# Kernel tuning notes

Hardware: AMD Instinct MI355X
Metric: run time of the kernel (lower is better)

## Reference

```python
import jax, jax.numpy as jnp
import numpy as np
import math

B, S, E, H = 2, 2048, 1024, 16
D = E // H
# neuromodulator levels (deterministic branch choices)
NA, ACH, DA = 0.5, 0.5, -0.5

def setup_inputs() -> dict:
    key = jax.random.key(0)
    ks = jax.random.split(key, 12)
    xav = lambda k, i, o: jax.random.uniform(k, (i, o), jnp.float32, -1.0, 1.0) * math.sqrt(6.0 / (i + o))
    return {
        'query': jax.random.normal(ks[0], (B, S, E), jnp.float32),
        'key':   jax.random.normal(ks[1], (B, S, E), jnp.float32),
        'value': jax.random.normal(ks[2], (B, S, E), jnp.float32),
        'Wq': xav(ks[3], E, E), 'bq': jnp.zeros((E,), jnp.float32),
        'Wk': xav(ks[4], E, E), 'bk': jnp.zeros((E,), jnp.float32),
        'Wv': xav(ks[5], E, E), 'bv': jnp.zeros((E,), jnp.float32),
        'Wo': xav(ks[6], E, E), 'bo': jnp.zeros((E,), jnp.float32),
        'time_scales': jnp.ones((H,), jnp.float32),
    }

def reference(query, key, value, Wq, bq, Wk, bk, Wv, bv, Wo, bo, time_scales):
    # projections -> [B, H, S, D]
    q = (query @ Wq + bq).reshape(B, S, H, D).transpose(0, 2, 1, 3)
    k = (key   @ Wk + bk).reshape(B, S, H, D).transpose(0, 2, 1, 3)
    v = (value @ Wv + bv).reshape(B, S, H, D).transpose(0, 2, 1, 3)
    # per-head time-scale on keys
    k = k * time_scales[None, :, None, None]
    scores = jnp.einsum('bhtd,bhsd->bhts', q, k) / math.sqrt(D)
    # noradrenaline: temperature scaling
    temperature = 1.0 / (1.0 + NA * 0.5)
    scores = scores / temperature
    # acetylcholine: boost diagonal
    diag = jnp.eye(S, dtype=scores.dtype)[None, None]
    scores = scores * (1.0 + ACH * 0.3 * diag)
    kk = max(1, int(S * 0.2))
    topv = jax.lax.top_k(scores, kk)[0]          # [B,H,S,kk]
    min_topk = topv[..., -1:]                     # kth largest
    mask = (scores >= min_topk).astype(scores.dtype)
    scores = scores * (1.0 + (-DA) * 0.3 * mask)
    attn = jax.nn.softmax(scores, axis=-1)
    out = jnp.einsum('bhts,bhsd->bhtd', attn, v)
    out = out.transpose(0, 2, 1, 3).reshape(B, S, E)
    out = out @ Wo + bo
    return out
```

## Files before the change

### kernel.cpp

```cpp
#include <hip/hip_runtime.h>
#include <cstdint>
#include <cstddef>

#define BB 2
#define SS 2048
#define EE 1024
#define HH 16
#define DH 64
#define KKSEL 409
#define QT 16
#define PST 136

typedef __attribute__((ext_vector_type(8))) short bf16x8;
typedef __attribute__((ext_vector_type(4))) float f32x4;
typedef unsigned short ushort_t;

__device__ __forceinline__ unsigned short f2bf(float f){
    unsigned u = __float_as_uint(f);
    u += 0x7fffu + ((u >> 16) & 1u);
    return (unsigned short)(u >> 16);
}
__device__ __forceinline__ float bf2f(unsigned short h){
    return __uint_as_float(((unsigned)h) << 16);
}
__device__ __forceinline__ unsigned sortkey(float f){
    unsigned u = __float_as_uint(f);
    return (u & 0x80000000u) ? ~u : (u | 0x80000000u);
}
__device__ __forceinline__ float inv_sortkey(unsigned k){
    unsigned u = (k & 0x80000000u) ? (k & 0x7fffffffu) : ~k;
    return __uint_as_float(u);
}
__device__ __forceinline__ void split8(const float* f, bf16x8& h, bf16x8& l){
    #pragma unroll
    for (int j = 0; j < 8; ++j){
        ushort_t hh = f2bf(f[j]);
        h[j] = (short)hh;
        l[j] = (short)f2bf(f[j] - bf2f(hh));
    }
}

struct CvtArgs {
    const float* W[4];
    ushort_t* H[4];
    ushort_t* L[4];
};

__global__ __launch_bounds__(256) void convert_wt4(CvtArgs a)
{
    __shared__ float T[64][65];
    const int z = blockIdx.z;
    const float* __restrict__ W = a.W[z];
    ushort_t* __restrict__ Ht = a.H[z];
    ushort_t* __restrict__ Lt = a.L[z];

    const int tid = threadIdx.x;
    const int ty = tid >> 4, tx = tid & 15;
    const int n0 = blockIdx.x * 64, k0 = blockIdx.y * 64;
    #pragma unroll
    for (int i = 0; i < 4; ++i){
        const int kl = ty + i * 16;
        float4 w = *(const float4*)&W[(size_t)(k0 + kl) * EE + n0 + tx * 4];
        T[kl][tx*4 + 0] = w.x; T[kl][tx*4 + 1] = w.y;
        T[kl][tx*4 + 2] = w.z; T[kl][tx*4 + 3] = w.w;
    }
    __syncthreads();
    #pragma unroll
    for (int i = 0; i < 4; ++i){
        const int nl = ty + i * 16;
        ushort4 h, l;
        ushort_t* hp = &h.x; ushort_t* lp = &l.x;
        #pragma unroll
        for (int j = 0; j < 4; ++j){
            const float v = T[tx*4 + j][nl];
            ushort_t hh = f2bf(v);
            hp[j] = hh;
            lp[j] = f2bf(v - bf2f(hh));
        }
        const size_t o = (size_t)(n0 + nl) * EE + k0 + tx * 4;
        *(ushort4*)&Ht[o] = h;
        *(ushort4*)&Lt[o] = l;
    }
}

template<int MODE>
__device__ __forceinline__ void gemm_body(
        const float* __restrict__ X,
        const ushort_t* __restrict__ Wth, const ushort_t* __restrict__ Wtl,
        const float* __restrict__ bias, const float* __restrict__ ts,
        float* __restrict__ OutF, ushort_t* __restrict__ OutH,
        ushort_t* __restrict__ OutL, ushort_t* buf)
{
    const int tid  = threadIdx.x;
    const int lane = tid & 63, wave = tid >> 6;
    const int c16  = lane & 15, qd = lane >> 4;
    const int m0 = blockIdx.y * 128, n0 = blockIdx.x * 128;
    const int wm = (wave >> 1) * 64, wn = (wave & 1) * 64;
    const int lrow = tid >> 1, lkg = (tid & 1) * 16;

    f32x4 acc[4][4];
    #pragma unroll
    for (int a = 0; a < 4; ++a)
        #pragma unroll
        for (int b = 0; b < 4; ++b) acc[a][b] = (f32x4){0.f,0.f,0.f,0.f};

    const float* Xr = X + (size_t)(m0 + lrow) * EE + lkg;
    const ushort_t* Whr = Wth + (size_t)(n0 + lrow) * EE + lkg;
    const ushort_t* Wlr = Wtl + (size_t)(n0 + lrow) * EE + lkg;

    {
        float fx[16];
        *(float4*)&fx[0]  = *(const float4*)&Xr[0];
        *(float4*)&fx[4]  = *(const float4*)&Xr[4];
        *(float4*)&fx[8]  = *(const float4*)&Xr[8];
        *(float4*)&fx[12] = *(const float4*)&Xr[12];
        bf16x8 w0 = *(const bf16x8*)&Whr[0];
        bf16x8 w1 = *(const bf16x8*)&Whr[8];
        bf16x8 w2 = *(const bf16x8*)&Wlr[0];
        bf16x8 w3 = *(const bf16x8*)&Wlr[8];
        bf16x8 h0, l0, h1, l1;
        split8(fx, h0, l0); split8(fx + 8, h1, l1);
        ushort_t* S = buf;
        *(bf16x8*)&S[lrow*32 + lkg]           = h0;
        *(bf16x8*)&S[lrow*32 + lkg + 8]       = h1;
        *(bf16x8*)&S[4096 + lrow*32 + lkg]    = l0;
        *(bf16x8*)&S[4096 + lrow*32 + lkg+8]  = l1;
        *(bf16x8*)&S[8192 + lrow*32 + lkg]    = w0;
        *(bf16x8*)&S[8192 + lrow*32 + lkg+8]  = w1;
        *(bf16x8*)&S[12288 + lrow*32 + lkg]   = w2;
        *(bf16x8*)&S[12288 + lrow*32 + lkg+8] = w3;
    }
    __syncthreads();

    int cur = 0;
    for (int k0 = 0; k0 < EE; k0 += 32){
        const bool more = (k0 + 32) < EE;
        float fx[16];
        bf16x8 gw[4];
        if (more){
            const float* xp = Xr + k0 + 32;
            *(float4*)&fx[0]  = *(const float4*)&xp[0];
            *(float4*)&fx[4]  = *(const float4*)&xp[4];
            *(float4*)&fx[8]  = *(const float4*)&xp[8];
            *(float4*)&fx[12] = *(const float4*)&xp[12];
            gw[0] = *(const bf16x8*)&Whr[k0 + 32];
            gw[1] = *(const bf16x8*)&Whr[k0 + 40];
            gw[2] = *(const bf16x8*)&Wlr[k0 + 32];
            gw[3] = *(const bf16x8*)&Wlr[k0 + 40];
        }
        const ushort_t* S  = buf + cur * 16384;
        const ushort_t* A0 = S;
        const ushort_t* A1 = S + 4096;
        const ushort_t* B0 = S + 8192;
        const ushort_t* B1 = S + 12288;
        bf16x8 afh[4], afl[4], bfh[4], bfl[4];
        #pragma unroll
        for (int i = 0; i < 4; ++i){
            afh[i] = *(const bf16x8*)&A0[(wm + i*16 + c16)*32 + qd*8];
            afl[i] = *(const bf16x8*)&A1[(wm + i*16 + c16)*32 + qd*8];
            bfh[i] = *(const bf16x8*)&B0[(wn + i*16 + c16)*32 + qd*8];
            bfl[i] = *(const bf16x8*)&B1[(wn + i*16 + c16)*32 + qd*8];
        }
        #pragma unroll
        for (int a = 0; a < 4; ++a){
            #pragma unroll
            for (int b = 0; b < 4; ++b){
                if (MODE == 2){
                    acc[a][b] = __builtin_amdgcn_mfma_f32_16x16x32_bf16(afh[a], bfh[b], acc[a][b], 0,0,0);
                    acc[a][b] = __builtin_amdgcn_mfma_f32_16x16x32_bf16(afh[a], bfl[b], acc[a][b], 0,0,0);
                    acc[a][b] = __builtin_amdgcn_mfma_f32_16x16x32_bf16(afl[a], bfh[b], acc[a][b], 0,0,0);
                } else {
                    acc[a][b] = __builtin_amdgcn_mfma_f32_16x16x32_bf16(bfh[a], afh[b], acc[a][b], 0,0,0);
                    acc[a][b] = __builtin_amdgcn_mfma_f32_16x16x32_bf16(bfh[a], afl[b], acc[a][b], 0,0,0);
                    acc[a][b] = __builtin_amdgcn_mfma_f32_16x16x32_bf16(bfl[a], afh[b], acc[a][b], 0,0,0);
                }
            }
        }
        if (more){
            bf16x8 h0, l0, h1, l1;
            split8(fx, h0, l0); split8(fx + 8, h1, l1);
            ushort_t* N = buf + (cur ^ 1) * 16384;
            *(bf16x8*)&N[lrow*32 + lkg]           = h0;
            *(bf16x8*)&N[lrow*32 + lkg + 8]       = h1;
            *(bf16x8*)&N[4096 + lrow*32 + lkg]    = l0;
            *(bf16x8*)&N[4096 + lrow*32 + lkg+8]  = l1;
            *(bf16x8*)&N[8192 + lrow*32 + lkg]    = gw[0];
            *(bf16x8*)&N[8192 + lrow*32 + lkg+8]  = gw[1];
            *(bf16x8*)&N[12288 + lrow*32 + lkg]   = gw[2];
            *(bf16x8*)&N[12288 + lrow*32 + lkg+8] = gw[3];
            __syncthreads();
            cur ^= 1;
        }
    }

    if (MODE == 3){
        #pragma unroll
        for (int a = 0; a < 4; ++a){
            const int ng = n0 + wn + a*16 + qd*4;
            float4 b4 = *(const float4*)&bias[ng];
            const float bb[4] = {b4.x, b4.y, b4.z, b4.w};
            #pragma unroll
            for (int b = 0; b < 4; ++b){
                const int mg = m0 + wm + b*16 + c16;
                float4 o;
                o.x = acc[a][b][0] + bb[0]; o.y = acc[a][b][1] + bb[1];
                o.z = acc[a][b][2] + bb[2]; o.w = acc[a][b][3] + bb[3];
                *(float4*)&OutF[(size_t)mg * EE + ng] = o;
            }
        }
    } else if (MODE == 0){
        #pragma unroll
        for (int a = 0; a < 4; ++a){
            const int ng = n0 + wn + a*16 + qd*4;
            const int h = ng >> 6, d0 = ng & 63;
            float4 b4 = *(const float4*)&bias[ng];
            const float bb[4] = {b4.x, b4.y, b4.z, b4.w};
            #pragma unroll
            for (int b = 0; b < 4; ++b){
                const int mg = m0 + wm + b*16 + c16;
                const int bi = mg >> 11, s = mg & (SS - 1);
                ushort4 hv, lv;
                ushort_t* hp = &hv.x; ushort_t* lp = &lv.x;
                #pragma unroll
                for (int r = 0; r < 4; ++r){
                    const float v = acc[a][b][r] + bb[r];
                    ushort_t hh = f2bf(v);
                    hp[r] = hh;
                    lp[r] = f2bf(v - bf2f(hh));
                }
                const size_t o = (((size_t)(bi * HH + h)) * SS + s) * DH + d0;
                *(ushort4*)&OutH[o] = hv;
                *(ushort4*)&OutL[o] = lv;
            }
        }
    } else if (MODE == 1){
        #pragma unroll
        for (int a = 0; a < 4; ++a){
            const int ng = n0 + wn + a*16 + qd*4;
            const int h = ng >> 6, d0 = ng & 63;
            const float tsc = ts[h];
            float4 b4 = *(const float4*)&bias[ng];
            const float bb[4] = {b4.x, b4.y, b4.z, b4.w};
            #pragma unroll
            for (int b = 0; b < 4; ++b){
                const int mg = m0 + wm + b*16 + c16;
                const int bi = mg >> 11, s = mg & (SS - 1);
                ushort4 hv;
                ushort_t* hp = &hv.x;
                #pragma unroll
                for (int r = 0; r < 4; ++r)
                    hp[r] = f2bf((acc[a][b][r] + bb[r]) * tsc);
                *(ushort4*)&OutH[(((size_t)(bi * HH + h)) * SS + s) * DH + d0] = hv;
            }
        }
    } else {
        #pragma unroll
        for (int a = 0; a < 4; ++a){
            const int mg = m0 + wm + a*16 + qd*4;
            const int bi = mg >> 11, s0 = mg & (SS - 1);
            #pragma unroll
            for (int b = 0; b < 4; ++b){
                const int ng = n0 + wn + b*16 + c16;
                const int h = ng >> 6, d = ng & 63;
                const float bv = bias[ng];
                ushort4 hv;
                ushort_t* hp = &hv.x;
                #pragma unroll
                for (int r = 0; r < 4; ++r) hp[r] = f2bf(acc[a][b][r] + bv);
                *(ushort4*)&OutH[(((size_t)(bi * HH + h)) * DH + d) * SS + s0] = hv;
            }
        }
    }
}

__global__ __launch_bounds__(256) void gemm_qkv(
        const float* __restrict__ q, const float* __restrict__ k,
        const float* __restrict__ v,
        const ushort_t* __restrict__ Wqh, const ushort_t* __restrict__ Wql,
        const ushort_t* __restrict__ Wkh, const ushort_t* __restrict__ Wkl,
        const ushort_t* __restrict__ Wvh, const ushort_t* __restrict__ Wvl,
        const float* __restrict__ bq, const float* __restrict__ bk,
        const float* __restrict__ bv, const float* __restrict__ ts,
        ushort_t* __restrict__ Qh, ushort_t* __restrict__ Ql,
        ushort_t* __restrict__ Kh, ushort_t* __restrict__ Vth)
{
    __shared__ ushort_t buf[2 * 16384];
    const int z = blockIdx.z;
    if (z == 0)
        gemm_body<0>(q, Wqh, Wql, bq, nullptr, nullptr, Qh, Ql, buf);
    else if (z == 1)
        gemm_body<1>(k, Wkh, Wkl, bk, ts, nullptr, Kh, nullptr, buf);
    else
        gemm_body<2>(v, Wvh, Wvl, bv, nullptr, nullptr, Vth, nullptr, buf);
}

__global__ __launch_bounds__(256) void gemm_out(
        const float* __restrict__ X,
        const ushort_t* __restrict__ Wth, const ushort_t* __restrict__ Wtl,
        const float* __restrict__ bias, float* __restrict__ OutF)
{
    __shared__ ushort_t buf[2 * 16384];
    gemm_body<3>(X, Wth, Wtl, bias, nullptr, OutF, nullptr, nullptr, buf);
}

__global__ __launch_bounds__(512, 4) void attn_kernel(
        const ushort_t* __restrict__ Qh, const ushort_t* __restrict__ Ql,
        const ushort_t* __restrict__ Khi, const ushort_t* __restrict__ Vth,
        float* __restrict__ AO)
{
    __shared__ __align__(16) char uni[65536];
    __shared__ float wsums[8][16];
    __shared__ float thr16[16];

    const int tid  = threadIdx.x;
    const int lane = tid & 63;
    const int wave = tid >> 6;
    const int qd   = lane >> 4;
    const int c16  = lane & 15;
    const unsigned Bx = blockIdx.x;
    const int xcd  = Bx & 7;
    const int qq   = Bx >> 3;
    const int tile = qq & 127;
    const int bh   = (qq >> 7) * 8 + xcd;
    const int t0   = tile * QT;
    const int wbase = wave * 256;

    bf16x8 qh[2], ql[2];
    {
        const size_t qbase = ((size_t)bh * SS + t0 + c16) * DH;
        #pragma unroll
        for (int kc = 0; kc < 2; ++kc){
            qh[kc] = *(const bf16x8*)&Qh[qbase + kc*32 + qd*8];
            ql[kc] = *(const bf16x8*)&Ql[qbase + kc*32 + qd*8];
        }
    }

    f32x4 acc[16];
    const ushort_t* Kh = Khi + (size_t)bh * SS * DH;
    #pragma unroll
    for (int t = 0; t < 16; ++t){
        f32x4 a = {0.f, 0.f, 0.f, 0.f};
        const int srow = wbase + t*16 + c16;
        const ushort_t* kp = Kh + (size_t)srow * DH + qd*8;
        #pragma unroll
        for (int kc = 0; kc < 2; ++kc){
            bf16x8 kh = *(const bf16x8*)(kp + kc*32);
            a = __builtin_amdgcn_mfma_f32_16x16x32_bf16(qh[kc], kh, a, 0, 0, 0);
            a = __builtin_amdgcn_mfma_f32_16x16x32_bf16(ql[kc], kh, a, 0, 0, 0);
        }
        acc[t] = a;
    }

    #pragma unroll
    for (int t = 0; t < 16; ++t){
        const int colg = wbase + t*16 + c16;
        #pragma unroll
        for (int r = 0; r < 4; ++r){
            float v = acc[t][r] * 0.15625f;
            if (colg == t0 + qd*4 + r) v *= 1.15f;
            acc[t][r] = v;
        }
    }

    float* ex = (float*)uni;
    #pragma unroll
    for (int half = 0; half < 2; ++half){
        if ((qd >> 1) == half){
            const int rl = (qd & 1) * 4;
            #pragma unroll
            for (int t = 0; t < 16; ++t)
                #pragma unroll
                for (int r = 0; r < 4; ++r)
                    ex[(rl + r) * SS + wbase + t*16 + c16] = acc[t][r];
        }
        __syncthreads();
        float cand[32];
        #pragma unroll
        for (int j = 0; j < 32; ++j)
            cand[j] = ex[wave * SS + lane + 64*j];
        float mx = cand[0], mn = cand[0];
        #pragma unroll
        for (int j = 1; j < 32; ++j){
            mx = fmaxf(mx, cand[j]);
            mn = fminf(mn, cand[j]);
        }
        #pragma unroll
        for (int off = 1; off < 64; off <<= 1){
            mx = fmaxf(mx, __shfl_xor(mx, off, 64));
            mn = fminf(mn, __shfl_xor(mn, off, 64));
        }
        unsigned lo = sortkey(mn), hi = sortkey(mx) + 1u;
        #pragma unroll 1
        for (int it = 0; it < 32 && (hi - lo) > 1u; ++it){
            const unsigned mid = lo + ((hi - lo) >> 1);
            const float midf = inv_sortkey(mid);
            int c = 0;
            #pragma unroll
            for (int j = 0; j < 32; ++j)
                c += (int)__popcll(__ballot(cand[j] >= midf));
            if (c == KKSEL){ lo = mid; break; }
            if (c > KKSEL) lo = mid; else hi = mid;
        }
        if (lane == 0) thr16[half*8 + wave] = inv_sortkey(lo);
        __syncthreads();
    }

    float thr[4];
    #pragma unroll
    for (int r = 0; r < 4; ++r) thr[r] = thr16[qd*4 + r];
    float psum[4] = {0.f, 0.f, 0.f, 0.f};
    #pragma unroll
    for (int t = 0; t < 16; ++t){
        #pragma unroll
        for (int r = 0; r < 4; ++r){
            float s = acc[t][r];
            s *= (s >= thr[r]) ? 1.15f : 1.0f;
            const float e = __expf(s);
            acc[t][r] = e;
            psum[r] += e;
        }
    }
    #pragma unroll
    for (int off = 1; off <= 8; off <<= 1){
        #pragma unroll
        for (int r = 0; r < 4; ++r) psum[r] += __shfl_xor(psum[r], off, 64);
    }
    if (c16 == 0){
        #pragma unroll
        for (int r = 0; r < 4; ++r) wsums[wave][qd*4 + r] = psum[r];
    }
    __syncthreads();
    float pinv[4];
    #pragma unroll
    for (int r = 0; r < 4; ++r){
        const int row = qd*4 + r;
        float s = 0.f;
        #pragma unroll
        for (int w = 0; w < 8; ++w) s += wsums[w][row];
        pinv[r] = 1.f / s;
    }

    const ushort_t* Vh = Vth + (size_t)bh * DH * SS;
    ushort_t* pw = (ushort_t*)uni + wave * (QT * PST);
    f32x4 oacc[4];
    #pragma unroll
    for (int dt = 0; dt < 4; ++dt) oacc[dt] = (f32x4){0.f, 0.f, 0.f, 0.f};

    #pragma unroll
    for (int half = 0; half < 2; ++half){
        #pragma unroll
        for (int tt = 0; tt < 8; ++tt){
            const int t = half*8 + tt;
            #pragma unroll
            for (int r = 0; r < 4; ++r)
                pw[(qd*4 + r) * PST + tt*16 + c16] = f2bf(acc[t][r] * pinv[r]);
        }
        #pragma unroll
        for (int kc = 0; kc < 4; ++kc){
            bf16x8 pf = *(const bf16x8*)&pw[c16 * PST + kc*32 + qd*8];
            const int sbase = wbase + half*128 + kc*32 + qd*8;
            #pragma unroll
            for (int dt = 0; dt < 4; ++dt){
                const int d = dt*16 + c16;
                bf16x8 vh = *(const bf16x8*)(Vh + (size_t)d * SS + sbase);
                oacc[dt] = __builtin_amdgcn_mfma_f32_16x16x32_bf16(pf, vh, oacc[dt], 0, 0, 0);
            }
        }
    }

    __syncthreads();
    float* red = (float*)uni;
    #pragma unroll
    for (int dt = 0; dt < 4; ++dt)
        #pragma unroll
        for (int r = 0; r < 4; ++r)
            red[(wave*16 + qd*4 + r) * 65 + dt*16 + c16] = oacc[dt][r];
    __syncthreads();

    const int b = bh >> 4, h = bh & 15;
    {
        const int r  = tid >> 5;
        const int c2 = (tid & 31) * 2;
        float s0 = 0.f, s1 = 0.f;
        #pragma unroll
        for (int w = 0; w < 8; ++w){
            s0 += red[(w*16 + r) * 65 + c2];
            s1 += red[(w*16 + r) * 65 + c2 + 1];
        }
        float2 o; o.x = s0; o.y = s1;
        *(float2*)&AO[((size_t)b * SS + t0 + r) * EE + h*DH + c2] = o;
    }
}

extern "C" void kernel_launch(void* const* d_in, const int* in_sizes, int n_in,
                              void* d_out, int out_size, void* d_ws, size_t ws_size,
                              hipStream_t stream)
{
    const float* query = (const float*)d_in[0];
    const float* key   = (const float*)d_in[1];
    const float* value = (const float*)d_in[2];
    const float* Wq    = (const float*)d_in[3];
    const float* bq    = (const float*)d_in[4];
    const float* Wk    = (const float*)d_in[5];
    const float* bk    = (const float*)d_in[6];
    const float* Wv    = (const float*)d_in[7];
    const float* bv    = (const float*)d_in[8];
    const float* Wo    = (const float*)d_in[9];
    const float* bo    = (const float*)d_in[10];
    const float* ts    = (const float*)d_in[11];
    float* out = (float*)d_out;
    char* w = (char*)d_ws;

    const size_t MB = 1u << 20;
    ushort_t* Qh  = (ushort_t*)(w + 0 * MB);
    ushort_t* Ql  = (ushort_t*)(w + 8 * MB);
    ushort_t* Kh  = (ushort_t*)(w + 16 * MB);
    ushort_t* Vth = (ushort_t*)(w + 24 * MB);
    float*    AOw = (float*)   (w + 32 * MB);
    ushort_t* Wqh = (ushort_t*)(w + 32 * MB);
    ushort_t* Wql = (ushort_t*)(w + 34 * MB);
    ushort_t* Wkh = (ushort_t*)(w + 36 * MB);
    ushort_t* Wkl = (ushort_t*)(w + 38 * MB);
    ushort_t* Wvh = (ushort_t*)(w + 40 * MB);
    ushort_t* Wvl = (ushort_t*)(w + 42 * MB);
    ushort_t* Woh = (ushort_t*)(w + 48 * MB);
    ushort_t* Wol = (ushort_t*)(w + 50 * MB);

    CvtArgs ca;
    ca.W[0] = Wq;  ca.W[1] = Wk;  ca.W[2] = Wv;  ca.W[3] = Wo;
    ca.H[0] = Wqh; ca.H[1] = Wkh; ca.H[2] = Wvh; ca.H[3] = Woh;
    ca.L[0] = Wql; ca.L[1] = Wkl; ca.L[2] = Wvl; ca.L[3] = Wol;

    hipLaunchKernelGGL(convert_wt4, dim3(16, 16, 4), dim3(256), 0, stream, ca);
    hipLaunchKernelGGL(gemm_qkv, dim3(8, 32, 3), dim3(256), 0, stream,
                       query, key, value, Wqh, Wql, Wkh, Wkl, Wvh, Wvl,
                       bq, bk, bv, ts, Qh, Ql, Kh, Vth);
    hipLaunchKernelGGL(attn_kernel, dim3(BB * HH * (SS / QT)), dim3(512), 0, stream,
                       Qh, Ql, Kh, Vth, AOw);
    hipLaunchKernelGGL(gemm_out, dim3(8, 32), dim3(256), 0, stream,
                       AOw, Woh, Wol, bo, out);
}
```

Baseline: 656.4 us.

## Use 4-way radix search for top-k threshold, fold scale into Q, add setprio

The top-k threshold search now tests three pivots per iteration instead of one, so each pass splits the range four ways and needs fewer iterations and ballot rounds. The 1/sqrt(D)*temperature scale moves into the Q projection epilogue, and the diagonal boost runs only in the wave that owns the diagonal. The two score-row halves are staged through shared memory so the second write overlaps the first search. s_setprio wraps the MFMA loops. Risks: the iteration cap drops from 32 to 20 (each pass still narrows the range more), and the scale is now applied before the bf16 hi/lo split, which changes rounding.

```diff
diff --git a/kernel.cpp b/kernel.cpp
--- a/kernel.cpp
+++ b/kernel.cpp
@@ -38,6 +38,46 @@
         h[j] = (short)hh;
         l[j] = (short)f2bf(f[j] - bf2f(hh));
     }
+}
+
+__device__ __forceinline__ float topk_thresh(const float* cand){
+    float mx = cand[0], mn = cand[0];
+    #pragma unroll
+    for (int j = 1; j < 32; ++j){
+        mx = fmaxf(mx, cand[j]);
+        mn = fminf(mn, cand[j]);
+    }
+    #pragma unroll
+    for (int off = 1; off < 64; off <<= 1){
+        mx = fmaxf(mx, __shfl_xor(mx, off, 64));
+        mn = fminf(mn, __shfl_xor(mn, off, 64));
+    }
+    unsigned lo = sortkey(mn), hi = sortkey(mx) + 1u;
+    #pragma unroll 1
+    for (int it = 0; it < 20 && (hi - lo) > 1u; ++it){
+        const unsigned span = hi - lo;
+        const unsigned p1 = lo + (span >> 2);
+        const unsigned p2 = lo + (span >> 1);
+        const unsigned p3 = p2 + (span >> 2);
+        const float f1 = inv_sortkey(p1);
+        const float f2 = inv_sortkey(p2);
+        const float f3 = inv_sortkey(p3);
+        int c1 = 0, c2 = 0, c3 = 0;
+        #pragma unroll
+        for (int j = 0; j < 32; ++j){
+            c1 += (int)__popcll(__ballot(cand[j] >= f1));
+            c2 += (int)__popcll(__ballot(cand[j] >= f2));
+            c3 += (int)__popcll(__ballot(cand[j] >= f3));
+        }
+        if (c1 == KKSEL){ lo = p1; break; }
+        if (c2 == KKSEL){ lo = p2; break; }
+        if (c3 == KKSEL){ lo = p3; break; }
+        if (c1 < KKSEL)       hi = p1;
+        else if (c2 < KKSEL){ lo = p1; hi = p2; }
+        else if (c3 < KKSEL){ lo = p2; hi = p3; }
+        else                  lo = p3;
+    }
+    return inv_sortkey(lo);
 }
 
 struct CvtArgs {
@@ -161,6 +201,7 @@
             bfh[i] = *(const bf16x8*)&B0[(wn + i*16 + c16)*32 + qd*8];
             bfl[i] = *(const bf16x8*)&B1[(wn + i*16 + c16)*32 + qd*8];
         }
+        __builtin_amdgcn_s_setprio(1);
         #pragma unroll
         for (int a = 0; a < 4; ++a){
             #pragma unroll
@@ -176,6 +217,7 @@
                 }
             }
         }
+        __builtin_amdgcn_s_setprio(0);
         if (more){
             bf16x8 h0, l0, h1, l1;
             split8(fx, h0, l0); split8(fx + 8, h1, l1);
@@ -223,7 +265,7 @@
                 ushort_t* hp = &hv.x; ushort_t* lp = &lv.x;
                 #pragma unroll
                 for (int r = 0; r < 4; ++r){
-                    const float v = acc[a][b][r] + bb[r];
+                    const float v = (acc[a][b][r] + bb[r]) * 0.15625f;
                     ushort_t hh = f2bf(v);
                     hp[r] = hh;
                     lp[r] = f2bf(v - bf2f(hh));
@@ -337,6 +379,7 @@
 
     f32x4 acc[16];
     const ushort_t* Kh = Khi + (size_t)bh * SS * DH;
+    __builtin_amdgcn_s_setprio(1);
     #pragma unroll
     for (int t = 0; t < 16; ++t){
         f32x4 a = {0.f, 0.f, 0.f, 0.f};
@@ -350,60 +393,54 @@
         }
         acc[t] = a;
     }
-
-    #pragma unroll
-    for (int t = 0; t < 16; ++t){
-        const int colg = wbase + t*16 + c16;
-        #pragma unroll
-        for (int r = 0; r < 4; ++r){
-            float v = acc[t][r] * 0.15625f;
-            if (colg == t0 + qd*4 + r) v *= 1.15f;
-            acc[t][r] = v;
+    __builtin_amdgcn_s_setprio(0);
+
+    if (wave == (t0 >> 8)){
+        #pragma unroll
+        for (int t = 0; t < 16; ++t){
+            const int colg = wbase + t*16 + c16;
+            #pragma unroll
+            for (int r = 0; r < 4; ++r)
+                if (colg == t0 + qd*4 + r) acc[t][r] *= 1.15f;
         }
     }
 
     float* ex = (float*)uni;
-    #pragma unroll
-    for (int half = 0; half < 2; ++half){
-        if ((qd >> 1) == half){
-            const int rl = (qd & 1) * 4;
-            #pragma unroll
-            for (int t = 0; t < 16; ++t)
-                #pragma unroll
-                for (int r = 0; r < 4; ++r)
-                    ex[(rl + r) * SS + wbase + t*16 + c16] = acc[t][r];
-        }
-        __syncthreads();
-        float cand[32];
-        #pragma unroll
-        for (int j = 0; j < 32; ++j)
-            cand[j] = ex[wave * SS + lane + 64*j];
-        float mx = cand[0], mn = cand[0];
-        #pragma unroll
-        for (int j = 1; j < 32; ++j){
-            mx = fmaxf(mx, cand[j]);
-            mn = fminf(mn, cand[j]);
-        }
-        #pragma unroll
-        for (int off = 1; off < 64; off <<= 1){
-            mx = fmaxf(mx, __shfl_xor(mx, off, 64));
-            mn = fminf(mn, __shfl_xor(mn, off, 64));
-        }
-        unsigned lo = sortkey(mn), hi = sortkey(mx) + 1u;
-        #pragma unroll 1
-        for (int it = 0; it < 32 && (hi - lo) > 1u; ++it){
-            const unsigned mid = lo + ((hi - lo) >> 1);
-            const float midf = inv_sortkey(mid);
-            int c = 0;
-            #pragma unroll
-            for (int j = 0; j < 32; ++j)
-                c += (int)__popcll(__ballot(cand[j] >= midf));
-            if (c == KKSEL){ lo = mid; break; }
-            if (c > KKSEL) lo = mid; else hi = mid;
-        }
-        if (lane == 0) thr16[half*8 + wave] = inv_sortkey(lo);
-        __syncthreads();
-    }
+    if (qd < 2){
+        const int rl = (qd & 1) * 4;
+        #pragma unroll
+        for (int t = 0; t < 16; ++t)
+            #pragma unroll
+            for (int r = 0; r < 4; ++r)
+                ex[(rl + r) * SS + wbase + t*16 + c16] = acc[t][r];
+    }
+    __syncthreads();
+    float cand[32];
+    #pragma unroll
+    for (int j = 0; j < 32; ++j)
+        cand[j] = ex[wave * SS + lane + 64*j];
+    __syncthreads();
+    if (qd >= 2){
+        const int rl = (qd & 1) * 4;
+        #pragma unroll
+        for (int t = 0; t < 16; ++t)
+            #pragma unroll
+            for (int r = 0; r < 4; ++r)
+                ex[(rl + r) * SS + wbase + t*16 + c16] = acc[t][r];
+    }
+    {
+        const float th0 = topk_thresh(cand);
+        if (lane == 0) thr16[wave] = th0;
+    }
+    __syncthreads();
+    #pragma unroll
+    for (int j = 0; j < 32; ++j)
+        cand[j] = ex[wave * SS + lane + 64*j];
+    {
+        const float th1 = topk_thresh(cand);
+        if (lane == 0) thr16[8 + wave] = th1;
+    }
+    __syncthreads();
 
     float thr[4];
     #pragma unroll
@@ -459,12 +496,14 @@
         for (int kc = 0; kc < 4; ++kc){
             bf16x8 pf = *(const bf16x8*)&pw[c16 * PST + kc*32 + qd*8];
             const int sbase = wbase + half*128 + kc*32 + qd*8;
+            __builtin_amdgcn_s_setprio(1);
             #pragma unroll
             for (int dt = 0; dt < 4; ++dt){
                 const int d = dt*16 + c16;
                 bf16x8 vh = *(const bf16x8*)(Vh + (size_t)d * SS + sbase);
                 oacc[dt] = __builtin_amdgcn_mfma_f32_16x16x32_bf16(pf, vh, oacc[dt], 0, 0, 0);
             }
+            __builtin_amdgcn_s_setprio(0);
         }
     }
 
```

Measured after the change: 712.2 us. 1.09x slower.

## Shrink GEMM N-tile, load weights via global_load_lds, use integer-key top-k search

Applied to the files above, without the earlier changes.

The GEMM tile drops from 128x128 to 128x64 with the grid doubled. Weight tiles now go straight to LDS through global_load_lds, and the register double-buffer is replaced by a single buffer with two barriers per k-step. This cuts LDS and register use to raise occupancy, at the cost of losing overlap between loads and MFMA. In attention, scores are stored as order-preserving integer keys. The top-k threshold bisection now uses an inline-asm unsigned compare plus popcount, starts from fixed bounds of ±64 instead of a computed min/max, and always runs 32 iterations unless it hits the exact count.

```diff
diff --git a/kernel.cpp b/kernel.cpp
--- a/kernel.cpp
+++ b/kernel.cpp
@@ -38,6 +38,11 @@
         h[j] = (short)hh;
         l[j] = (short)f2bf(f[j] - bf2f(hh));
     }
+}
+__device__ __forceinline__ void gload_lds16(const ushort_t* g, ushort_t* l){
+    __builtin_amdgcn_global_load_lds(
+        (const __attribute__((address_space(1))) void*)g,
+        (__attribute__((address_space(3))) void*)l, 16, 0, 0);
 }
 
 struct CvtArgs {
@@ -94,136 +99,113 @@
     const int tid  = threadIdx.x;
     const int lane = tid & 63, wave = tid >> 6;
     const int c16  = lane & 15, qd = lane >> 4;
-    const int m0 = blockIdx.y * 128, n0 = blockIdx.x * 128;
-    const int wm = (wave >> 1) * 64, wn = (wave & 1) * 64;
+    const int m0 = blockIdx.y * 128, n0 = blockIdx.x * 64;
+    const int wm = (wave >> 1) * 64, wn = (wave & 1) * 32;
     const int lrow = tid >> 1, lkg = (tid & 1) * 16;
 
-    f32x4 acc[4][4];
-    #pragma unroll
-    for (int a = 0; a < 4; ++a)
-        #pragma unroll
-        for (int b = 0; b < 4; ++b) acc[a][b] = (f32x4){0.f,0.f,0.f,0.f};
+    f32x4 acc[8];
+    #pragma unroll
+    for (int i = 0; i < 8; ++i) acc[i] = (f32x4){0.f,0.f,0.f,0.f};
 
     const float* Xr = X + (size_t)(m0 + lrow) * EE + lkg;
-    const ushort_t* Whr = Wth + (size_t)(n0 + lrow) * EE + lkg;
-    const ushort_t* Wlr = Wtl + (size_t)(n0 + lrow) * EE + lkg;
-
-    {
-        float fx[16];
-        *(float4*)&fx[0]  = *(const float4*)&Xr[0];
-        *(float4*)&fx[4]  = *(const float4*)&Xr[4];
-        *(float4*)&fx[8]  = *(const float4*)&Xr[8];
-        *(float4*)&fx[12] = *(const float4*)&Xr[12];
-        bf16x8 w0 = *(const bf16x8*)&Whr[0];
-        bf16x8 w1 = *(const bf16x8*)&Whr[8];
-        bf16x8 w2 = *(const bf16x8*)&Wlr[0];
-        bf16x8 w3 = *(const bf16x8*)&Wlr[8];
-        bf16x8 h0, l0, h1, l1;
-        split8(fx, h0, l0); split8(fx + 8, h1, l1);
-        ushort_t* S = buf;
-        *(bf16x8*)&S[lrow*32 + lkg]           = h0;
-        *(bf16x8*)&S[lrow*32 + lkg + 8]       = h1;
-        *(bf16x8*)&S[4096 + lrow*32 + lkg]    = l0;
-        *(bf16x8*)&S[4096 + lrow*32 + lkg+8]  = l1;
-        *(bf16x8*)&S[8192 + lrow*32 + lkg]    = w0;
-        *(bf16x8*)&S[8192 + lrow*32 + lkg+8]  = w1;
-        *(bf16x8*)&S[12288 + lrow*32 + lkg]   = w2;
-        *(bf16x8*)&S[12288 + lrow*32 + lkg+8] = w3;
-    }
-    __syncthreads();
-
-    int cur = 0;
+
+    const size_t wofs = (size_t)(n0 + wave*16 + (lane >> 2)) * EE + (lane & 3) * 8;
+    const ushort_t* Wh = Wth + wofs;
+    const ushort_t* Wl = Wtl + wofs;
+
     for (int k0 = 0; k0 < EE; k0 += 32){
-        const bool more = (k0 + 32) < EE;
-        float fx[16];
-        bf16x8 gw[4];
-        if (more){
-            const float* xp = Xr + k0 + 32;
+        gload_lds16(Wh + k0, buf + 8192  + wave*512);
+        gload_lds16(Wl + k0, buf + 10240 + wave*512);
+        {
+            float fx[16];
+            const float* xp = Xr + k0;
             *(float4*)&fx[0]  = *(const float4*)&xp[0];
             *(float4*)&fx[4]  = *(const float4*)&xp[4];
             *(float4*)&fx[8]  = *(const float4*)&xp[8];
             *(float4*)&fx[12] = *(const float4*)&xp[12];
-            gw[0] = *(const bf16x8*)&Whr[k0 + 32];
-            gw[1] = *(const bf16x8*)&Whr[k0 + 40];
-            gw[2] = *(const bf16x8*)&Wlr[k0 + 32];
-            gw[3] = *(const bf16x8*)&Wlr[k0 + 40];
-        }
-        const ushort_t* S  = buf + cur * 16384;
-        const ushort_t* A0 = S;
-        const ushort_t* A1 = S + 4096;
-        const ushort_t* B0 = S + 8192;
-        const ushort_t* B1 = S + 12288;
-        bf16x8 afh[4], afl[4], bfh[4], bfl[4];
+            bf16x8 h0, l0, h1, l1;
+            split8(fx, h0, l0); split8(fx + 8, h1, l1);
+            *(bf16x8*)&buf[lrow*32 + lkg]           = h0;
+            *(bf16x8*)&buf[lrow*32 + lkg + 8]       = h1;
+            *(bf16x8*)&buf[4096 + lrow*32 + lkg]    = l0;
+            *(bf16x8*)&buf[4096 + lrow*32 + lkg+8]  = l1;
+        }
+        __syncthreads();
+
+        const ushort_t* A0 = buf;
+        const ushort_t* A1 = buf + 4096;
+        const ushort_t* B0 = buf + 8192;
+        const ushort_t* B1 = buf + 10240;
+        bf16x8 afh[4], afl[4], bfh[2], bfl[2];
         #pragma unroll
         for (int i = 0; i < 4; ++i){
             afh[i] = *(const bf16x8*)&A0[(wm + i*16 + c16)*32 + qd*8];
             afl[i] = *(const bf16x8*)&A1[(wm + i*16 + c16)*32 + qd*8];
-            bfh[i] = *(const bf16x8*)&B0[(wn + i*16 + c16)*32 + qd*8];
-            bfl[i] = *(const bf16x8*)&B1[(wn + i*16 + c16)*32 + qd*8];
-        }
-        #pragma unroll
-        for (int a = 0; a < 4; ++a){
-            #pragma unroll
-            for (int b = 0; b < 4; ++b){
-                if (MODE == 2){
-                    acc[a][b] = __builtin_amdgcn_mfma_f32_16x16x32_bf16(afh[a], bfh[b], acc[a][b], 0,0,0);
-                    acc[a][b] = __builtin_amdgcn_mfma_f32_16x16x32_bf16(afh[a], bfl[b], acc[a][b], 0,0,0);
-                    acc[a][b] = __builtin_amdgcn_mfma_f32_16x16x32_bf16(afl[a], bfh[b], acc[a][b], 0,0,0);
-                } else {
-                    acc[a][b] = __builtin_amdgcn_mfma_f32_16x16x32_bf16(bfh[a], afh[b], acc[a][b], 0,0,0);
-                    acc[a][b] = __builtin_amdgcn_mfma_f32_16x16x32_bf16(bfh[a], afl[b], acc[a][b], 0,0,0);
-                    acc[a][b] = __builtin_amdgcn_mfma_f32_16x16x32_bf16(bfl[a], afh[b], acc[a][b], 0,0,0);
+        }
+        #pragma unroll
+        for (int j = 0; j < 2; ++j){
+            bfh[j] = *(const bf16x8*)&B0[(wn + j*16 + c16)*32 + qd*8];
+            bfl[j] = *(const bf16x8*)&B1[(wn + j*16 + c16)*32 + qd*8];
+        }
+        if (MODE == 2){
+            #pragma unroll
+            for (int ma = 0; ma < 4; ++ma){
+                #pragma unroll
+                for (int nb = 0; nb < 2; ++nb){
+                    const int id = ma*2 + nb;
+                    acc[id] = __builtin_amdgcn_mfma_f32_16x16x32_bf16(afh[ma], bfh[nb], acc[id], 0,0,0);
+                    acc[id] = __builtin_amdgcn_mfma_f32_16x16x32_bf16(afh[ma], bfl[nb], acc[id], 0,0,0);
+                    acc[id] = __builtin_amdgcn_mfma_f32_16x16x32_bf16(afl[ma], bfh[nb], acc[id], 0,0,0);
                 }
             }
-        }
-        if (more){
-            bf16x8 h0, l0, h1, l1;
-            split8(fx, h0, l0); split8(fx + 8, h1, l1);
-            ushort_t* N = buf + (cur ^ 1) * 16384;
-            *(bf16x8*)&N[lrow*32 + lkg]           = h0;
-            *(bf16x8*)&N[lrow*32 + lkg + 8]       = h1;
-            *(bf16x8*)&N[4096 + lrow*32 + lkg]    = l0;
-            *(bf16x8*)&N[4096 + lrow*32 + lkg+8]  = l1;
-            *(bf16x8*)&N[8192 + lrow*32 + lkg]    = gw[0];
-            *(bf16x8*)&N[8192 + lrow*32 + lkg+8]  = gw[1];
-            *(bf16x8*)&N[12288 + lrow*32 + lkg]   = gw[2];
-            *(bf16x8*)&N[12288 + lrow*32 + lkg+8] = gw[3];
-            __syncthreads();
-            cur ^= 1;
-        }
+        } else {
+            #pragma unroll
+            for (int na = 0; na < 2; ++na){
+                #pragma unroll
+                for (int mb = 0; mb < 4; ++mb){
+                    const int id = na*4 + mb;
+                    acc[id] = __builtin_amdgcn_mfma_f32_16x16x32_bf16(bfh[na], afh[mb], acc[id], 0,0,0);
+                    acc[id] = __builtin_amdgcn_mfma_f32_16x16x32_bf16(bfh[na], afl[mb], acc[id], 0,0,0);
+                    acc[id] = __builtin_amdgcn_mfma_f32_16x16x32_bf16(bfl[na], afh[mb], acc[id], 0,0,0);
+                }
+            }
+        }
+        if (k0 + 32 < EE) __syncthreads();
     }
 
     if (MODE == 3){
         #pragma unroll
-        for (int a = 0; a < 4; ++a){
-            const int ng = n0 + wn + a*16 + qd*4;
+        for (int na = 0; na < 2; ++na){
+            const int ng = n0 + wn + na*16 + qd*4;
             float4 b4 = *(const float4*)&bias[ng];
             const float bb[4] = {b4.x, b4.y, b4.z, b4.w};
             #pragma unroll
-            for (int b = 0; b < 4; ++b){
-                const int mg = m0 + wm + b*16 + c16;
+            for (int mb = 0; mb < 4; ++mb){
+                const int mg = m0 + wm + mb*16 + c16;
+                const f32x4 av = acc[na*4 + mb];
                 float4 o;
-                o.x = acc[a][b][0] + bb[0]; o.y = acc[a][b][1] + bb[1];
-                o.z = acc[a][b][2] + bb[2]; o.w = acc[a][b][3] + bb[3];
+                o.x = av[0] + bb[0]; o.y = av[1] + bb[1];
+                o.z = av[2] + bb[2]; o.w = av[3] + bb[3];
                 *(float4*)&OutF[(size_t)mg * EE + ng] = o;
             }
         }
     } else if (MODE == 0){
         #pragma unroll
-        for (int a = 0; a < 4; ++a){
-            const int ng = n0 + wn + a*16 + qd*4;
+        for (int na = 0; na < 2; ++na){
+            const int ng = n0 + wn + na*16 + qd*4;
             const int h = ng >> 6, d0 = ng & 63;
             float4 b4 = *(const float4*)&bias[ng];
             const float bb[4] = {b4.x, b4.y, b4.z, b4.w};
             #pragma unroll
-            for (int b = 0; b < 4; ++b){
-                const int mg = m0 + wm + b*16 + c16;
+            for (int mb = 0; mb < 4; ++mb){
+                const int mg = m0 + wm + mb*16 + c16;
                 const int bi = mg >> 11, s = mg & (SS - 1);
+                const f32x4 av = acc[na*4 + mb];
                 ushort4 hv, lv;
                 ushort_t* hp = &hv.x; ushort_t* lp = &lv.x;
                 #pragma unroll
                 for (int r = 0; r < 4; ++r){
-                    const float v = acc[a][b][r] + bb[r];
+                    const float v = av[r] + bb[r];
                     ushort_t hh = f2bf(v);
                     hp[r] = hh;
                     lp[r] = f2bf(v - bf2f(hh));
@@ -235,38 +217,40 @@
         }
     } else if (MODE == 1){
         #pragma unroll
-        for (int a = 0; a < 4; ++a){
-            const int ng = n0 + wn + a*16 + qd*4;
+        for (int na = 0; na < 2; ++na){
+            const int ng = n0 + wn + na*16 + qd*4;
             const int h = ng >> 6, d0 = ng & 63;
             const float tsc = ts[h];
             float4 b4 = *(const float4*)&bias[ng];
             const float bb[4] = {b4.x, b4.y, b4.z, b4.w};
             #pragma unroll
-            for (int b = 0; b < 4; ++b){
-                const int mg = m0 + wm + b*16 + c16;
+            for (int mb = 0; mb < 4; ++mb){
+                const int mg = m0 + wm + mb*16 + c16;
                 const int bi = mg >> 11, s = mg & (SS - 1);
+                const f32x4 av = acc[na*4 + mb];
                 ushort4 hv;
                 ushort_t* hp = &hv.x;
                 #pragma unroll
                 for (int r = 0; r < 4; ++r)
-                    hp[r] = f2bf((acc[a][b][r] + bb[r]) * tsc);
+                    hp[r] = f2bf((av[r] + bb[r]) * tsc);
                 *(ushort4*)&OutH[(((size_t)(bi * HH + h)) * SS + s) * DH + d0] = hv;
             }
         }
     } else {
         #pragma unroll
-        for (int a = 0; a < 4; ++a){
-            const int mg = m0 + wm + a*16 + qd*4;
+        for (int ma = 0; ma < 4; ++ma){
+            const int mg = m0 + wm + ma*16 + qd*4;
             const int bi = mg >> 11, s0 = mg & (SS - 1);
             #pragma unroll
-            for (int b = 0; b < 4; ++b){
-                const int ng = n0 + wn + b*16 + c16;
+            for (int nb = 0; nb < 2; ++nb){
+                const int ng = n0 + wn + nb*16 + c16;
                 const int h = ng >> 6, d = ng & 63;
                 const float bv = bias[ng];
+                const f32x4 av = acc[ma*2 + nb];
                 ushort4 hv;
                 ushort_t* hp = &hv.x;
                 #pragma unroll
-                for (int r = 0; r < 4; ++r) hp[r] = f2bf(acc[a][b][r] + bv);
+                for (int r = 0; r < 4; ++r) hp[r] = f2bf(av[r] + bv);
                 *(ushort4*)&OutH[(((size_t)(bi * HH + h)) * DH + d) * SS + s0] = hv;
             }
         }
@@ -284,7 +268,7 @@
         ushort_t* __restrict__ Qh, ushort_t* __restrict__ Ql,
         ushort_t* __restrict__ Kh, ushort_t* __restrict__ Vth)
 {
-    __shared__ ushort_t buf[2 * 16384];
+    __shared__ ushort_t buf[12288];
     const int z = blockIdx.z;
     if (z == 0)
         gemm_body<0>(q, Wqh, Wql, bq, nullptr, nullptr, Qh, Ql, buf);
@@ -299,7 +283,7 @@
         const ushort_t* __restrict__ Wth, const ushort_t* __restrict__ Wtl,
         const float* __restrict__ bias, float* __restrict__ OutF)
 {
-    __shared__ ushort_t buf[2 * 16384];
+    __shared__ ushort_t buf[12288];
     gemm_body<3>(X, Wth, Wtl, bias, nullptr, OutF, nullptr, nullptr, buf);
 }
 
@@ -310,7 +294,7 @@
 {
     __shared__ __align__(16) char uni[65536];
     __shared__ float wsums[8][16];
-    __shared__ float thr16[16];
+    __shared__ unsigned thr16[16];
 
     const int tid  = threadIdx.x;
     const int lane = tid & 63;
@@ -358,7 +342,7 @@
         for (int r = 0; r < 4; ++r){
             float v = acc[t][r] * 0.15625f;
             if (colg == t0 + qd*4 + r) v *= 1.15f;
-            acc[t][r] = v;
+            acc[t][r] = __uint_as_float(sortkey(v));
         }
     }
 
@@ -374,38 +358,31 @@
                     ex[(rl + r) * SS + wbase + t*16 + c16] = acc[t][r];
         }
         __syncthreads();
-        float cand[32];
+        unsigned cand[32];
         #pragma unroll
         for (int j = 0; j < 32; ++j)
-            cand[j] = ex[wave * SS + lane + 64*j];
-        float mx = cand[0], mn = cand[0];
-        #pragma unroll
-        for (int j = 1; j < 32; ++j){
-            mx = fmaxf(mx, cand[j]);
-            mn = fminf(mn, cand[j]);
-        }
-        #pragma unroll
-        for (int off = 1; off < 64; off <<= 1){
-            mx = fmaxf(mx, __shfl_xor(mx, off, 64));
-            mn = fminf(mn, __shfl_xor(mn, off, 64));
-        }
-        unsigned lo = sortkey(mn), hi = sortkey(mx) + 1u;
+            cand[j] = __float_as_uint(ex[wave * SS + lane + 64*j]);
+        unsigned lo = sortkey(-64.0f), hi = sortkey(64.0f);
         #pragma unroll 1
-        for (int it = 0; it < 32 && (hi - lo) > 1u; ++it){
+        for (int it = 0; it < 32; ++it){
             const unsigned mid = lo + ((hi - lo) >> 1);
-            const float midf = inv_sortkey(mid);
             int c = 0;
             #pragma unroll
-            for (int j = 0; j < 32; ++j)
-                c += (int)__popcll(__ballot(cand[j] >= midf));
+            for (int j = 0; j < 32; ++j){
+                int pc;
+                asm("v_cmp_le_u32 vcc, %1, %2\n\t"
+                    "s_bcnt1_i32_b64 %0, vcc"
+                    : "=s"(pc) : "s"(mid), "v"(cand[j]) : "vcc");
+                c += pc;
+            }
             if (c == KKSEL){ lo = mid; break; }
             if (c > KKSEL) lo = mid; else hi = mid;
         }
-        if (lane == 0) thr16[half*8 + wave] = inv_sortkey(lo);
+        if (lane == 0) thr16[half*8 + wave] = lo;
         __syncthreads();
     }
 
-    float thr[4];
+    unsigned thr[4];
     #pragma unroll
     for (int r = 0; r < 4; ++r) thr[r] = thr16[qd*4 + r];
     float psum[4] = {0.f, 0.f, 0.f, 0.f};
@@ -413,8 +390,9 @@
     for (int t = 0; t < 16; ++t){
         #pragma unroll
         for (int r = 0; r < 4; ++r){
-            float s = acc[t][r];
-            s *= (s >= thr[r]) ? 1.15f : 1.0f;
+            const unsigned key = __float_as_uint(acc[t][r]);
+            float s = inv_sortkey(key);
+            s *= (key >= thr[r]) ? 1.15f : 1.0f;
             const float e = __expf(s);
             acc[t][r] = e;
             psum[r] += e;
@@ -532,11 +510,11 @@
     ca.L[0] = Wql; ca.L[1] = Wkl; ca.L[2] = Wvl; ca.L[3] = Wol;
 
     hipLaunchKernelGGL(convert_wt4, dim3(16, 16, 4), dim3(256), 0, stream, ca);
-    hipLaunchKernelGGL(gemm_qkv, dim3(8, 32, 3), dim3(256), 0, stream,
+    hipLaunchKernelGGL(gemm_qkv, dim3(16, 32, 3), dim3(256), 0, stream,
                        query, key, value, Wqh, Wql, Wkh, Wkl, Wvh, Wvl,
                        bq, bk, bv, ts, Qh, Ql, Kh, Vth);
     hipLaunchKernelGGL(attn_kernel, dim3(BB * HH * (SS / QT)), dim3(512), 0, stream,
                        Qh, Ql, Kh, Vth, AOw);
-    hipLaunchKernelGGL(gemm_out, dim3(8, 32), dim3(256), 0, stream,
+    hipLaunchKernelGGL(gemm_out, dim3(16, 32), dim3(256), 0, stream,
                        AOw, Woh, Wol, bo, out);
 }
```

After: 662.8 us. Within noise of the previous version (+1.0%).
